# Performance work log

Measured on AMD Instinct MI355X. Metric: run time of the kernel, lower is better.

Reference implementation:

```python
import jax, jax.numpy as jnp
import numpy as np

MAX_REL = 32
NPE = 16
NRBF = 16
KNN = 32

def _layer_norm(x, g, b, eps=1e-5):
    mu = jnp.mean(x, axis=-1, keepdims=True)
    var = jnp.mean((x - mu) ** 2, axis=-1, keepdims=True)
    return (x - mu) * jax.lax.rsqrt(var + eps) * g + b

def _forward(dist_ca, omega, theta, phi, dihedral, mask_angle, mask, S, residue_idx, chain_encoding_all, pos_W, pos_b, edge_W, ln_e_g, ln_e_b, embed_tab, node_W, node_b, ln_n_g, ln_n_b):
    B, L, _ = dist_ca.shape
    # kNN graph from masked CA distances (smallest-K, ascending -> matches torch.topk largest=False)
    D = mask_angle * dist_ca
    D_max = jnp.max(D, axis=-1, keepdims=True)
    D_adjust = D + (1.0 - mask_angle) * D_max
    neg_vals, E_idx = jax.lax.top_k(-D_adjust, KNN)
    D_neighbors = -neg_vals                                     # [B,L,K]
    # 7 pairwise scalar edge channels, gathered at neighbor indices
    offset = (residue_idx[:, :, None] - residue_idx[:, None, :]).astype(jnp.float32)
    feats = jnp.stack([offset, jnp.cos(omega), jnp.sin(omega), jnp.cos(theta), jnp.sin(theta), jnp.cos(phi), jnp.sin(phi)], axis=0)  # [7,B,L,L]
    gathered = jnp.take_along_axis(feats, E_idx[None], axis=3)  # [7,B,L,K]
    edge_s = jax.lax.stop_gradient(gathered).astype(jnp.int32)  # torch .long(): truncate toward zero
    same_chain = (chain_encoding_all[:, :, None] == chain_encoding_all[:, None, :]).astype(jnp.int32)
    E_chains = jnp.take_along_axis(same_chain, E_idx, axis=2)[None]  # [1,B,L,K], broadcasts like tile(7,1,1)
    d = jnp.clip(edge_s + MAX_REL, 0, 2 * MAX_REL) * E_chains + (1 - E_chains) * (2 * MAX_REL + 1)
    E_pos = pos_W[d] + pos_b                                    # one_hot(d,66) @ W == row gather; [7,B,L,K,NPE]
    # rearrange '(n b) l t c -> b l t (n c)'
    E_pos = jnp.transpose(E_pos, (1, 2, 3, 0, 4)).reshape(B, L, KNN, 7 * NPE)
    # RBF of neighbor distances
    mu = jnp.linspace(2.0, 22.0, NRBF)
    sigma = (22.0 - 2.0) / NRBF
    RBF = jnp.exp(-(((D_neighbors[..., None] - mu) / sigma) ** 2))  # [B,L,K,NRBF]
    E = jnp.concatenate([E_pos, RBF], axis=-1) @ edge_W          # [B,L,K,128]
    E = _layer_norm(E, ln_e_g, ln_e_b)
    # node features: embedding(22->6) cat dihedral(6) -> linear(12->128) -> LN
    V = jnp.concatenate([embed_tab[S], dihedral], axis=-1) @ node_W + node_b
    V = _layer_norm(V, ln_n_g, ln_n_b)
    return V, E, E_idx

def setup_inputs():
    key = jax.random.key(0)
    ks = jax.random.split(key, 12)
    B, L, EF = 4, 2048, 128
    inp = {}
    inp["dist_ca"] = jax.random.uniform(ks[0], (B, L, L), jnp.float32) * 20.0 + 2.0
    inp["omega"] = jax.random.normal(ks[1], (B, L, L), jnp.float32)
    inp["theta"] = jax.random.normal(ks[2], (B, L, L), jnp.float32)
    inp["phi"] = jax.random.normal(ks[3], (B, L, L), jnp.float32)
    inp["dihedral"] = jax.random.normal(ks[4], (B, L, 6), jnp.float32)
    inp["mask_angle"] = jnp.ones((B, L, L), jnp.float32)
    inp["mask"] = jnp.ones((B, L), jnp.float32)
    inp["S"] = jax.random.randint(ks[5], (B, L), 0, 22)
    inp["residue_idx"] = jnp.arange(B * L, dtype=jnp.int32).reshape(B, L)
    inp["chain_encoding_all"] = jax.random.randint(ks[6], (B, L), 0, 4)
    # learned parameters (torch Linear weight transposed to [in,out])
    inp["pos_W"] = jax.random.normal(ks[7], (2 * MAX_REL + 2, NPE), jnp.float32) * 0.05
    inp["pos_b"] = jnp.zeros((NPE,), jnp.float32)
    inp["edge_W"] = jax.random.normal(ks[8], (7 * NPE + NRBF, EF), jnp.float32) * 0.05
    inp["ln_e_g"] = jnp.ones((EF,), jnp.float32)
    inp["ln_e_b"] = jnp.zeros((EF,), jnp.float32)
    inp["embed_tab"] = (jax.random.normal(ks[9], (22, 6), jnp.float32) * 0.5).at[21].set(0.0)  # padding_idx=21
    inp["node_W"] = jax.random.normal(ks[10], (12, EF), jnp.float32) * 0.1
    inp["node_b"] = jnp.zeros((EF,), jnp.float32)
    inp["ln_n_g"] = jnp.ones((EF,), jnp.float32)
    inp["ln_n_b"] = jnp.zeros((EF,), jnp.float32)
    return inp

def reference(dist_ca, omega, theta, phi, dihedral, mask_angle, mask, S, residue_idx, chain_encoding_all, pos_W, pos_b, edge_W, ln_e_g, ln_e_b, embed_tab, node_W, node_b, ln_n_g, ln_n_b):
    return _forward(dist_ca, omega, theta, phi, dihedral, mask_angle, mask, S, residue_idx, chain_encoding_all, pos_W, pos_b, edge_W, ln_e_g, ln_e_b, embed_tab, node_W, node_b, ln_n_g, ln_n_b)
```

## Files before the change

kernel.cpp:

```cpp
#include <hip/hip_runtime.h>
#include <hip/hip_bf16.h>
#include <math.h>

namespace {
constexpr int Ln   = 2048;
constexpr int Kn   = 32;
constexpr int EFn  = 128;
constexpr int ROWS = 4 * Ln;
constexpr size_t V_ELEMS = (size_t)ROWS * EFn;
constexpr size_t E_ELEMS = (size_t)ROWS * Kn * EFn;
constexpr size_t IDX_OFF = V_ELEMS + E_ELEMS;

__device__ __forceinline__ unsigned int orderKey(float f) {
  unsigned int u = __float_as_uint(f);
  return (u & 0x80000000u) ? ~u : (u | 0x80000000u);
}
__device__ __forceinline__ float keyToFloat(unsigned int k) {
  unsigned int u = (k & 0x80000000u) ? (k & 0x7fffffffu) : ~k;
  return __uint_as_float(u);
}
__device__ __forceinline__ unsigned long long u64min(unsigned long long a, unsigned long long b) {
  return a < b ? a : b;
}
}

__global__ void pf_tab(const float* __restrict__ pos_W, const float* __restrict__ pos_b,
                       const float* __restrict__ edge_W, float* __restrict__ T) {
  int n = blockIdx.x / 66, dd = blockIdx.x % 66, c = threadIdx.x;
  float acc = 0.f;
#pragma unroll
  for (int m = 0; m < 16; m++)
    acc += (pos_W[dd * 16 + m] + pos_b[m]) * edge_W[(n * 16 + m) * EFn + c];
  T[(size_t)(n * 66 + dd) * EFn + c] = acc;
}

__global__ __launch_bounds__(256) void pf_main(
    const float* __restrict__ dist_ca, const float* __restrict__ omega,
    const float* __restrict__ theta, const float* __restrict__ phi,
    const float* __restrict__ dihedral, const float* __restrict__ mask_angle,
    const int* __restrict__ Sarr, const int* __restrict__ ridx,
    const int* __restrict__ chain, const float* __restrict__ T,
    const float* __restrict__ edge_W, const float* __restrict__ ln_e_g,
    const float* __restrict__ ln_e_b, const float* __restrict__ embed_tab,
    const float* __restrict__ node_W, const float* __restrict__ node_b,
    const float* __restrict__ ln_n_g, const float* __restrict__ ln_n_b,
    float* __restrict__ out) {
  __shared__ unsigned int s_keys[Ln];
  __shared__ unsigned int s_hist[256];
  __shared__ unsigned long long s_cand[64];
  __shared__ unsigned long long s_w64[4];
  __shared__ float s_mx[4], s_mn2[4], s_mx2[4];
  __shared__ float s_v4[4];
  __shared__ int s_nidx[Kn];
  __shared__ float s_nval[Kn];
  __shared__ int s_d7[Kn * 8];
  __shared__ int s_bsel, s_tot, s_cnt;

  const int tid = threadIdx.x;
  const int lane = tid & 63, wid = tid >> 6;
  const int r = blockIdx.x;
  const int b = r >> 11;
  const size_t rowoff = (size_t)r * Ln;

  float Dv[8], Mv[8];
  float lmax = -3.4e38f;
#pragma unroll
  for (int m = 0; m < 8; m++) {
    int j = tid + (m << 8);
    float mk = mask_angle[rowoff + j];
    float dd = mk * dist_ca[rowoff + j];
    Dv[m] = dd; Mv[m] = mk;
    lmax = fmaxf(lmax, dd);
  }
#pragma unroll
  for (int o = 32; o; o >>= 1) lmax = fmaxf(lmax, __shfl_xor(lmax, o));
  if (!lane) s_mx[wid] = lmax;
  __syncthreads();
  const float Dmax = fmaxf(fmaxf(s_mx[0], s_mx[1]), fmaxf(s_mx[2], s_mx[3]));

  float lmin = 3.4e38f; lmax = -3.4e38f;
#pragma unroll
  for (int m = 0; m < 8; m++) {
    float adj = Dv[m] + (1.0f - Mv[m]) * Dmax;
    Dv[m] = adj;
    s_keys[tid + (m << 8)] = orderKey(adj);
    lmin = fminf(lmin, adj); lmax = fmaxf(lmax, adj);
  }
#pragma unroll
  for (int o = 32; o; o >>= 1) {
    lmin = fminf(lmin, __shfl_xor(lmin, o));
    lmax = fmaxf(lmax, __shfl_xor(lmax, o));
  }
  if (!lane) { s_mn2[wid] = lmin; s_mx2[wid] = lmax; }
  s_hist[tid] = 0u;
  __syncthreads();
  const float m0 = fminf(fminf(s_mn2[0], s_mn2[1]), fminf(s_mn2[2], s_mn2[3]));
  const float M0 = fmaxf(fmaxf(s_mx2[0], s_mx2[1]), fmaxf(s_mx2[2], s_mx2[3]));
  const float rng = M0 - m0;
  const float scale = (rng > 0.f) ? 255.0f / rng : 0.f;

  int binv[8];
#pragma unroll
  for (int m = 0; m < 8; m++) {
    int bin = (int)((Dv[m] - m0) * scale);
    bin = bin < 0 ? 0 : (bin > 255 ? 255 : bin);
    binv[m] = bin;
    atomicAdd(&s_hist[bin], 1u);
  }
  __syncthreads();
  for (int off = 1; off < 256; off <<= 1) {
    unsigned int u = 0;
    if (tid >= off) u = s_hist[tid - off];
    __syncthreads();
    if (tid >= off) s_hist[tid] += u;
    __syncthreads();
  }
  {
    unsigned int cum = s_hist[tid];
    unsigned int cump = tid ? s_hist[tid - 1] : 0u;
    if (cum >= (unsigned)Kn && cump < (unsigned)Kn) { s_bsel = tid; s_tot = (int)cum; }
    if (!tid) s_cnt = 0;
  }
  __syncthreads();
  const int bsel = s_bsel;
  const int tot = s_tot;

  if (tot <= 64) {
#pragma unroll
    for (int m = 0; m < 8; m++) {
      if (binv[m] <= bsel) {
        int p = atomicAdd(&s_cnt, 1);
        s_cand[p] = ((unsigned long long)orderKey(Dv[m]) << 16) | (unsigned)(tid + (m << 8));
      }
    }
  }
  __syncthreads();

  if (tot <= 64) {
    if (tid < 64) {
      unsigned long long v = (tid < tot) ? s_cand[tid] : ~0ull;
#pragma unroll
      for (int size = 2; size <= 64; size <<= 1) {
        for (int stride = size >> 1; stride > 0; stride >>= 1) {
          unsigned long long p = __shfl_xor(v, stride);
          bool keepMin = (((tid & stride) == 0) == ((tid & size) == 0));
          v = ((v < p) != keepMin) ? p : v;
        }
      }
      if (tid < Kn) {
        s_nidx[tid] = (int)(v & 0xffffull);
        s_nval[tid] = keyToFloat((unsigned int)(v >> 16));
      }
    }
  } else {
    for (int t = 0; t < Kn; t++) {
      unsigned long long lm = ~0ull;
#pragma unroll
      for (int m = 0; m < 8; m++) {
        int j = tid + (m << 8);
        unsigned long long kk = ((unsigned long long)s_keys[j] << 16) | (unsigned)j;
        lm = u64min(lm, kk);
      }
#pragma unroll
      for (int o = 32; o; o >>= 1) lm = u64min(lm, __shfl_xor(lm, o));
      if (!lane) s_w64[wid] = lm;
      __syncthreads();
      unsigned long long g = u64min(u64min(s_w64[0], s_w64[1]), u64min(s_w64[2], s_w64[3]));
      int j = (int)(g & 0xffffull);
      if (tid == (j & 255)) s_keys[j] = 0xffffffffu;
      if (!tid) { s_nidx[t] = j; s_nval[t] = keyToFloat((unsigned int)(g >> 16)); }
      __syncthreads();
    }
  }
  __syncthreads();

  if (tid < Kn)
    out[IDX_OFF + (size_t)r * Kn + tid] = (float)s_nidx[tid];

  const int ri_i = ridx[r];
  const int ch_i = chain[r];
  if (tid < Kn) {
    int j = s_nidx[tid];
    int rj = ridx[(size_t)b * Ln + j];
    int sc = (ch_i == chain[(size_t)b * Ln + j]) ? 1 : 0;
    int e0 = (int)((float)(ri_i - rj));
    int d0 = e0 + 32; d0 = d0 < 0 ? 0 : (d0 > 64 ? 64 : d0);
    s_d7[tid * 8 + 0] = sc ? d0 : 65;
    size_t pij = rowoff + j;
    float om = omega[pij], th = theta[pij], ph = phi[pij];
    float vals[6] = { cosf(om), sinf(om), cosf(th), sinf(th), cosf(ph), sinf(ph) };
#pragma unroll
    for (int n = 0; n < 6; n++) {
      int e = (int)vals[n];
      int d = e + 32; d = d < 0 ? 0 : (d > 64 ? 64 : d);
      s_d7[tid * 8 + 1 + n] = sc ? d : 65;
    }
  }
  __syncthreads();

  {
    const int k = tid >> 3, sub = tid & 7, c0 = sub << 4;
    float acc[16];
    {
      const float* Tp = T + (size_t)s_d7[k * 8 + 0] * EFn + c0;
#pragma unroll
      for (int m = 0; m < 16; m++) acc[m] = Tp[m];
    }
#pragma unroll
    for (int n = 1; n < 7; n++) {
      const float* Tp = T + (size_t)(n * 66 + s_d7[k * 8 + n]) * EFn + c0;
#pragma unroll
      for (int m = 0; m < 16; m++) acc[m] += Tp[m];
    }
    const float dv = s_nval[k];
#pragma unroll
    for (int rr = 0; rr < 16; rr++) {
      float mu = 2.0f + (20.0f / 15.0f) * (float)rr;
      float t = (dv - mu) * 0.8f;
      float rb = expf(-t * t);
      const float* W2 = edge_W + (size_t)(112 + rr) * EFn + c0;
#pragma unroll
      for (int m = 0; m < 16; m++) acc[m] = fmaf(rb, W2[m], acc[m]);
    }
    float s1 = 0.f, s2 = 0.f;
#pragma unroll
    for (int m = 0; m < 16; m++) { s1 += acc[m]; s2 += acc[m] * acc[m]; }
#pragma unroll
    for (int o = 1; o < 8; o <<= 1) { s1 += __shfl_xor(s1, o); s2 += __shfl_xor(s2, o); }
    const float mean = s1 * (1.0f / 128.0f);
    float var = s2 * (1.0f / 128.0f) - mean * mean;
    var = fmaxf(var, 0.f);
    const float inv = rsqrtf(var + 1e-5f);
    float y[16];
#pragma unroll
    for (int m = 0; m < 16; m++)
      y[m] = (acc[m] - mean) * inv * ln_e_g[c0 + m] + ln_e_b[c0 + m];
    float4* dst = (float4*)(out + V_ELEMS + ((size_t)(r * Kn + k) * EFn + c0));
    dst[0] = make_float4(y[0],  y[1],  y[2],  y[3]);
    dst[1] = make_float4(y[4],  y[5],  y[6],  y[7]);
    dst[2] = make_float4(y[8],  y[9],  y[10], y[11]);
    dst[3] = make_float4(y[12], y[13], y[14], y[15]);
  }

  float a = 0.f;
  if (tid < EFn) {
    const int c = tid;
    const int sv = Sarr[r];
    a = node_b[c];
#pragma unroll
    for (int m = 0; m < 6; m++) a = fmaf(embed_tab[sv * 6 + m], node_W[m * EFn + c], a);
#pragma unroll
    for (int m = 0; m < 6; m++) a = fmaf(dihedral[(size_t)r * 6 + m], node_W[(6 + m) * EFn + c], a);
    float s1 = a, s2 = a * a;
#pragma unroll
    for (int o = 32; o; o >>= 1) { s1 += __shfl_xor(s1, o); s2 += __shfl_xor(s2, o); }
    if (!lane) { s_v4[wid * 2] = s1; s_v4[wid * 2 + 1] = s2; }
  }
  __syncthreads();
  if (tid < EFn) {
    const float S1 = s_v4[0] + s_v4[2], S2 = s_v4[1] + s_v4[3];
    const float mean = S1 * (1.0f / 128.0f);
    float var = S2 * (1.0f / 128.0f) - mean * mean;
    var = fmaxf(var, 0.f);
    const float inv = rsqrtf(var + 1e-5f);
    const float yv = (a - mean) * inv * ln_n_g[tid] + ln_n_b[tid];
    out[(size_t)r * EFn + tid] = yv;
  }
}

extern "C" void kernel_launch(void* const* d_in, const int* in_sizes, int n_in,
                              void* d_out, int out_size, void* d_ws, size_t ws_size,
                              hipStream_t stream) {
  (void)in_sizes; (void)n_in; (void)out_size; (void)ws_size;
  const float* dist_ca    = (const float*)d_in[0];
  const float* omega      = (const float*)d_in[1];
  const float* theta      = (const float*)d_in[2];
  const float* phi        = (const float*)d_in[3];
  const float* dihedral   = (const float*)d_in[4];
  const float* mask_angle = (const float*)d_in[5];
  const int*   S          = (const int*)d_in[7];
  const int*   ridx       = (const int*)d_in[8];
  const int*   chain      = (const int*)d_in[9];
  const float* pos_W      = (const float*)d_in[10];
  const float* pos_b      = (const float*)d_in[11];
  const float* edge_W     = (const float*)d_in[12];
  const float* ln_e_g     = (const float*)d_in[13];
  const float* ln_e_b     = (const float*)d_in[14];
  const float* embed_tab  = (const float*)d_in[15];
  const float* node_W     = (const float*)d_in[16];
  const float* node_b     = (const float*)d_in[17];
  const float* ln_n_g     = (const float*)d_in[18];
  const float* ln_n_b     = (const float*)d_in[19];

  float* T = (float*)d_ws;

  pf_tab<<<7 * 66, 128, 0, stream>>>(pos_W, pos_b, edge_W, T);
  pf_main<<<ROWS, 256, 0, stream>>>(dist_ca, omega, theta, phi, dihedral, mask_angle,
                                    S, ridx, chain, T, edge_W, ln_e_g, ln_e_b,
                                    embed_tab, node_W, node_b, ln_n_g, ln_n_b,
                                    (float*)d_out);
}
```

Measured before the change: 513.3 us.

## Split fused kernel into top-k and edge-feature kernels with vectorized loads

Splits the single per-row kernel into a top-k/node kernel and a separate edge kernel. The top-k kernel hands neighbor metadata to the edge kernel through a packed workspace buffer. The top-k kernel now uses float4 loads, a wave-shuffle prefix scan in place of the barrier-heavy shared scan, and a register valid-mask in place of the shared key array, which cuts LDS use. The edge kernel spreads sin/cos across lanes, shares them by shuffle, and uses __expf. The trade-off is an extra launch, a global round trip for the metadata, and reduced exp precision.

```diff
diff --git a/kernel.cpp b/kernel.cpp
--- a/kernel.cpp
+++ b/kernel.cpp
@@ -10,6 +10,7 @@
 constexpr size_t V_ELEMS = (size_t)ROWS * EFn;
 constexpr size_t E_ELEMS = (size_t)ROWS * Kn * EFn;
 constexpr size_t IDX_OFF = V_ELEMS + E_ELEMS;
+constexpr size_t T_BYTES = (size_t)7 * 66 * EFn * 4;
 
 __device__ __forceinline__ unsigned int orderKey(float f) {
   unsigned int u = __float_as_uint(f);
@@ -34,26 +35,22 @@
   T[(size_t)(n * 66 + dd) * EFn + c] = acc;
 }
 
-__global__ __launch_bounds__(256) void pf_main(
-    const float* __restrict__ dist_ca, const float* __restrict__ omega,
-    const float* __restrict__ theta, const float* __restrict__ phi,
-    const float* __restrict__ dihedral, const float* __restrict__ mask_angle,
-    const int* __restrict__ Sarr, const int* __restrict__ ridx,
-    const int* __restrict__ chain, const float* __restrict__ T,
-    const float* __restrict__ edge_W, const float* __restrict__ ln_e_g,
-    const float* __restrict__ ln_e_b, const float* __restrict__ embed_tab,
-    const float* __restrict__ node_W, const float* __restrict__ node_b,
-    const float* __restrict__ ln_n_g, const float* __restrict__ ln_n_b,
-    float* __restrict__ out) {
-  __shared__ unsigned int s_keys[Ln];
+__global__ __launch_bounds__(256) void pf_topk(
+    const float* __restrict__ dist_ca, const float* __restrict__ mask_angle,
+    const float* __restrict__ dihedral, const int* __restrict__ Sarr,
+    const int* __restrict__ ridx, const int* __restrict__ chain,
+    const float* __restrict__ embed_tab, const float* __restrict__ node_W,
+    const float* __restrict__ node_b, const float* __restrict__ ln_n_g,
+    const float* __restrict__ ln_n_b,
+    uint2* __restrict__ ew, float* __restrict__ out) {
   __shared__ unsigned int s_hist[256];
+  __shared__ unsigned int s_wtot[4];
   __shared__ unsigned long long s_cand[64];
   __shared__ unsigned long long s_w64[4];
   __shared__ float s_mx[4], s_mn2[4], s_mx2[4];
   __shared__ float s_v4[4];
   __shared__ int s_nidx[Kn];
   __shared__ float s_nval[Kn];
-  __shared__ int s_d7[Kn * 8];
   __shared__ int s_bsel, s_tot, s_cnt;
 
   const int tid = threadIdx.x;
@@ -62,19 +59,26 @@
   const int b = r >> 11;
   const size_t rowoff = (size_t)r * Ln;
 
+  const int j0 = tid << 2;
+
   float Dv[8], Mv[8];
+  {
+    float4 da = *(const float4*)(dist_ca + rowoff + j0);
+    float4 db = *(const float4*)(dist_ca + rowoff + 1024 + j0);
+    float4 ma = *(const float4*)(mask_angle + rowoff + j0);
+    float4 mb = *(const float4*)(mask_angle + rowoff + 1024 + j0);
+    Mv[0] = ma.x; Mv[1] = ma.y; Mv[2] = ma.z; Mv[3] = ma.w;
+    Mv[4] = mb.x; Mv[5] = mb.y; Mv[6] = mb.z; Mv[7] = mb.w;
+    Dv[0] = ma.x * da.x; Dv[1] = ma.y * da.y; Dv[2] = ma.z * da.z; Dv[3] = ma.w * da.w;
+    Dv[4] = mb.x * db.x; Dv[5] = mb.y * db.y; Dv[6] = mb.z * db.z; Dv[7] = mb.w * db.w;
+  }
   float lmax = -3.4e38f;
 #pragma unroll
-  for (int m = 0; m < 8; m++) {
-    int j = tid + (m << 8);
-    float mk = mask_angle[rowoff + j];
-    float dd = mk * dist_ca[rowoff + j];
-    Dv[m] = dd; Mv[m] = mk;
-    lmax = fmaxf(lmax, dd);
-  }
+  for (int m = 0; m < 8; m++) lmax = fmaxf(lmax, Dv[m]);
 #pragma unroll
   for (int o = 32; o; o >>= 1) lmax = fmaxf(lmax, __shfl_xor(lmax, o));
   if (!lane) s_mx[wid] = lmax;
+  if (!tid) s_cnt = 0;
   __syncthreads();
   const float Dmax = fmaxf(fmaxf(s_mx[0], s_mx[1]), fmaxf(s_mx[2], s_mx[3]));
 
@@ -83,7 +87,6 @@
   for (int m = 0; m < 8; m++) {
     float adj = Dv[m] + (1.0f - Mv[m]) * Dmax;
     Dv[m] = adj;
-    s_keys[tid + (m << 8)] = orderKey(adj);
     lmin = fminf(lmin, adj); lmax = fmaxf(lmax, adj);
   }
 #pragma unroll
@@ -108,18 +111,24 @@
     atomicAdd(&s_hist[bin], 1u);
   }
   __syncthreads();
-  for (int off = 1; off < 256; off <<= 1) {
-    unsigned int u = 0;
-    if (tid >= off) u = s_hist[tid - off];
+
+  {
+    const unsigned int orig = s_hist[tid];
+    unsigned int v = orig;
+#pragma unroll
+    for (int o = 1; o < 64; o <<= 1) {
+      unsigned int u = __shfl_up(v, o);
+      if (lane >= o) v += u;
+    }
+    if (lane == 63) s_wtot[wid] = v;
     __syncthreads();
-    if (tid >= off) s_hist[tid] += u;
-    __syncthreads();
-  }
-  {
-    unsigned int cum = s_hist[tid];
-    unsigned int cump = tid ? s_hist[tid - 1] : 0u;
-    if (cum >= (unsigned)Kn && cump < (unsigned)Kn) { s_bsel = tid; s_tot = (int)cum; }
-    if (!tid) s_cnt = 0;
+    unsigned int add = 0;
+#pragma unroll
+    for (int w = 0; w < 4; w++) if (w < wid) add += s_wtot[w];
+    const unsigned int cum = v + add;
+    if (cum >= (unsigned)Kn && (cum - orig) < (unsigned)Kn) {
+      s_bsel = tid; s_tot = (int)cum;
+    }
   }
   __syncthreads();
   const int bsel = s_bsel;
@@ -130,13 +139,11 @@
     for (int m = 0; m < 8; m++) {
       if (binv[m] <= bsel) {
         int p = atomicAdd(&s_cnt, 1);
-        s_cand[p] = ((unsigned long long)orderKey(Dv[m]) << 16) | (unsigned)(tid + (m << 8));
+        int j = (m < 4) ? (j0 + m) : (1024 + j0 + m - 4);
+        s_cand[p] = ((unsigned long long)orderKey(Dv[m]) << 16) | (unsigned)j;
       }
     }
-  }
-  __syncthreads();
-
-  if (tot <= 64) {
+    __syncthreads();
     if (tid < 64) {
       unsigned long long v = (tid < tot) ? s_cand[tid] : ~0ull;
 #pragma unroll
@@ -153,13 +160,15 @@
       }
     }
   } else {
+    unsigned int valid = 0xffu;
     for (int t = 0; t < Kn; t++) {
       unsigned long long lm = ~0ull;
 #pragma unroll
       for (int m = 0; m < 8; m++) {
-        int j = tid + (m << 8);
-        unsigned long long kk = ((unsigned long long)s_keys[j] << 16) | (unsigned)j;
-        lm = u64min(lm, kk);
+        if (valid & (1u << m)) {
+          int j = (m < 4) ? (j0 + m) : (1024 + j0 + m - 4);
+          lm = u64min(lm, ((unsigned long long)orderKey(Dv[m]) << 16) | (unsigned)j);
+        }
       }
 #pragma unroll
       for (int o = 32; o; o >>= 1) lm = u64min(lm, __shfl_xor(lm, o));
@@ -167,90 +176,34 @@
       __syncthreads();
       unsigned long long g = u64min(u64min(s_w64[0], s_w64[1]), u64min(s_w64[2], s_w64[3]));
       int j = (int)(g & 0xffffull);
-      if (tid == (j & 255)) s_keys[j] = 0xffffffffu;
+      int owner = (j < 1024) ? (j >> 2) : ((j - 1024) >> 2);
+      if (tid == owner) valid &= ~(1u << ((j < 1024) ? (j & 3) : (4 + (j & 3))));
       if (!tid) { s_nidx[t] = j; s_nval[t] = keyToFloat((unsigned int)(g >> 16)); }
       __syncthreads();
     }
   }
   __syncthreads();
 
-  if (tid < Kn)
-    out[IDX_OFF + (size_t)r * Kn + tid] = (float)s_nidx[tid];
-
-  const int ri_i = ridx[r];
-  const int ch_i = chain[r];
   if (tid < Kn) {
     int j = s_nidx[tid];
+    out[IDX_OFF + (size_t)r * Kn + tid] = (float)j;
     int rj = ridx[(size_t)b * Ln + j];
-    int sc = (ch_i == chain[(size_t)b * Ln + j]) ? 1 : 0;
-    int e0 = (int)((float)(ri_i - rj));
-    int d0 = e0 + 32; d0 = d0 < 0 ? 0 : (d0 > 64 ? 64 : d0);
-    s_d7[tid * 8 + 0] = sc ? d0 : 65;
-    size_t pij = rowoff + j;
-    float om = omega[pij], th = theta[pij], ph = phi[pij];
-    float vals[6] = { cosf(om), sinf(om), cosf(th), sinf(th), cosf(ph), sinf(ph) };
-#pragma unroll
-    for (int n = 0; n < 6; n++) {
-      int e = (int)vals[n];
-      int d = e + 32; d = d < 0 ? 0 : (d > 64 ? 64 : d);
-      s_d7[tid * 8 + 1 + n] = sc ? d : 65;
-    }
-  }
-  __syncthreads();
-
-  {
-    const int k = tid >> 3, sub = tid & 7, c0 = sub << 4;
-    float acc[16];
-    {
-      const float* Tp = T + (size_t)s_d7[k * 8 + 0] * EFn + c0;
-#pragma unroll
-      for (int m = 0; m < 16; m++) acc[m] = Tp[m];
-    }
-#pragma unroll
-    for (int n = 1; n < 7; n++) {
-      const float* Tp = T + (size_t)(n * 66 + s_d7[k * 8 + n]) * EFn + c0;
-#pragma unroll
-      for (int m = 0; m < 16; m++) acc[m] += Tp[m];
-    }
-    const float dv = s_nval[k];
-#pragma unroll
-    for (int rr = 0; rr < 16; rr++) {
-      float mu = 2.0f + (20.0f / 15.0f) * (float)rr;
-      float t = (dv - mu) * 0.8f;
-      float rb = expf(-t * t);
-      const float* W2 = edge_W + (size_t)(112 + rr) * EFn + c0;
-#pragma unroll
-      for (int m = 0; m < 16; m++) acc[m] = fmaf(rb, W2[m], acc[m]);
-    }
-    float s1 = 0.f, s2 = 0.f;
-#pragma unroll
-    for (int m = 0; m < 16; m++) { s1 += acc[m]; s2 += acc[m] * acc[m]; }
-#pragma unroll
-    for (int o = 1; o < 8; o <<= 1) { s1 += __shfl_xor(s1, o); s2 += __shfl_xor(s2, o); }
-    const float mean = s1 * (1.0f / 128.0f);
-    float var = s2 * (1.0f / 128.0f) - mean * mean;
-    var = fmaxf(var, 0.f);
-    const float inv = rsqrtf(var + 1e-5f);
-    float y[16];
-#pragma unroll
-    for (int m = 0; m < 16; m++)
-      y[m] = (acc[m] - mean) * inv * ln_e_g[c0 + m] + ln_e_b[c0 + m];
-    float4* dst = (float4*)(out + V_ELEMS + ((size_t)(r * Kn + k) * EFn + c0));
-    dst[0] = make_float4(y[0],  y[1],  y[2],  y[3]);
-    dst[1] = make_float4(y[4],  y[5],  y[6],  y[7]);
-    dst[2] = make_float4(y[8],  y[9],  y[10], y[11]);
-    dst[3] = make_float4(y[12], y[13], y[14], y[15]);
+    int sc = (chain[r] == chain[(size_t)b * Ln + j]) ? 1 : 0;
+    int d0 = (ridx[r] - rj) + 32;
+    d0 = d0 < 0 ? 0 : (d0 > 64 ? 64 : d0);
+    d0 = sc ? d0 : 65;
+    unsigned int meta = (unsigned)j | ((unsigned)d0 << 11) | ((unsigned)sc << 18);
+    ew[(size_t)r * Kn + tid] = make_uint2(meta, __float_as_uint(s_nval[tid]));
   }
 
   float a = 0.f;
   if (tid < EFn) {
-    const int c = tid;
     const int sv = Sarr[r];
-    a = node_b[c];
-#pragma unroll
-    for (int m = 0; m < 6; m++) a = fmaf(embed_tab[sv * 6 + m], node_W[m * EFn + c], a);
-#pragma unroll
-    for (int m = 0; m < 6; m++) a = fmaf(dihedral[(size_t)r * 6 + m], node_W[(6 + m) * EFn + c], a);
+    a = node_b[tid];
+#pragma unroll
+    for (int m = 0; m < 6; m++) a = fmaf(embed_tab[sv * 6 + m], node_W[m * EFn + tid], a);
+#pragma unroll
+    for (int m = 0; m < 6; m++) a = fmaf(dihedral[(size_t)r * 6 + m], node_W[(6 + m) * EFn + tid], a);
     float s1 = a, s2 = a * a;
 #pragma unroll
     for (int o = 32; o; o >>= 1) { s1 += __shfl_xor(s1, o); s2 += __shfl_xor(s2, o); }
@@ -263,9 +216,82 @@
     float var = S2 * (1.0f / 128.0f) - mean * mean;
     var = fmaxf(var, 0.f);
     const float inv = rsqrtf(var + 1e-5f);
-    const float yv = (a - mean) * inv * ln_n_g[tid] + ln_n_b[tid];
-    out[(size_t)r * EFn + tid] = yv;
-  }
+    out[(size_t)r * EFn + tid] = (a - mean) * inv * ln_n_g[tid] + ln_n_b[tid];
+  }
+}
+
+__global__ __launch_bounds__(256) void pf_edge(
+    const uint2* __restrict__ ew, const float* __restrict__ omega,
+    const float* __restrict__ theta, const float* __restrict__ phi,
+    const float* __restrict__ T, const float* __restrict__ edge_W,
+    const float* __restrict__ ln_e_g, const float* __restrict__ ln_e_b,
+    float* __restrict__ out) {
+  const int tid = threadIdx.x;
+  const int e = blockIdx.x * 32 + (tid >> 3);
+  const int sub = tid & 7, c0 = sub << 4;
+
+  const uint2 md = ew[e];
+  const unsigned meta = md.x;
+  const float dval = __uint_as_float(md.y);
+  const int j = meta & 0x7ff;
+  const int d0 = (meta >> 11) & 0x7f;
+  const int sc = (meta >> 18) & 1;
+  const int r = e >> 5;
+
+  const size_t pij = (size_t)r * Ln + j;
+  float ang = 0.f;
+  if (sub == 0) ang = omega[pij];
+  else if (sub == 1) ang = theta[pij];
+  else if (sub == 2) ang = phi[pij];
+  const float cv = cosf(ang), sv = sinf(ang);
+  const int base = (tid & 63) & ~7;
+  float tr[6];
+  tr[0] = __shfl(cv, base + 0); tr[1] = __shfl(sv, base + 0);
+  tr[2] = __shfl(cv, base + 1); tr[3] = __shfl(sv, base + 1);
+  tr[4] = __shfl(cv, base + 2); tr[5] = __shfl(sv, base + 2);
+
+  float acc[16];
+  {
+    const float* Tp = T + (size_t)d0 * EFn + c0;
+#pragma unroll
+    for (int m = 0; m < 16; m++) acc[m] = Tp[m];
+  }
+#pragma unroll
+  for (int n = 1; n < 7; n++) {
+    int ee = (int)tr[n - 1];
+    int d = ee + 32; d = d < 0 ? 0 : (d > 64 ? 64 : d);
+    d = sc ? d : 65;
+    const float* Tp = T + (size_t)(n * 66 + d) * EFn + c0;
+#pragma unroll
+    for (int m = 0; m < 16; m++) acc[m] += Tp[m];
+  }
+#pragma unroll
+  for (int rr = 0; rr < 16; rr++) {
+    float mu = 2.0f + (20.0f / 15.0f) * (float)rr;
+    float t = (dval - mu) * 0.8f;
+    float rb = __expf(-t * t);
+    const float* W2 = edge_W + (size_t)(112 + rr) * EFn + c0;
+#pragma unroll
+    for (int m = 0; m < 16; m++) acc[m] = fmaf(rb, W2[m], acc[m]);
+  }
+  float s1 = 0.f, s2 = 0.f;
+#pragma unroll
+  for (int m = 0; m < 16; m++) { s1 += acc[m]; s2 += acc[m] * acc[m]; }
+#pragma unroll
+  for (int o = 1; o < 8; o <<= 1) { s1 += __shfl_xor(s1, o); s2 += __shfl_xor(s2, o); }
+  const float mean = s1 * (1.0f / 128.0f);
+  float var = s2 * (1.0f / 128.0f) - mean * mean;
+  var = fmaxf(var, 0.f);
+  const float inv = rsqrtf(var + 1e-5f);
+  float y[16];
+#pragma unroll
+  for (int m = 0; m < 16; m++)
+    y[m] = (acc[m] - mean) * inv * ln_e_g[c0 + m] + ln_e_b[c0 + m];
+  float4* dst = (float4*)(out + V_ELEMS + ((size_t)e * EFn + c0));
+  dst[0] = make_float4(y[0],  y[1],  y[2],  y[3]);
+  dst[1] = make_float4(y[4],  y[5],  y[6],  y[7]);
+  dst[2] = make_float4(y[8],  y[9],  y[10], y[11]);
+  dst[3] = make_float4(y[12], y[13], y[14], y[15]);
 }
 
 extern "C" void kernel_launch(void* const* d_in, const int* in_sizes, int n_in,
@@ -292,11 +318,13 @@
   const float* ln_n_g     = (const float*)d_in[18];
   const float* ln_n_b     = (const float*)d_in[19];
 
-  float* T = (float*)d_ws;
+  float* T  = (float*)d_ws;
+  uint2* ew = (uint2*)((char*)d_ws + T_BYTES);
 
   pf_tab<<<7 * 66, 128, 0, stream>>>(pos_W, pos_b, edge_W, T);
-  pf_main<<<ROWS, 256, 0, stream>>>(dist_ca, omega, theta, phi, dihedral, mask_angle,
-                                    S, ridx, chain, T, edge_W, ln_e_g, ln_e_b,
+  pf_topk<<<ROWS, 256, 0, stream>>>(dist_ca, mask_angle, dihedral, S, ridx, chain,
                                     embed_tab, node_W, node_b, ln_n_g, ln_n_b,
-                                    (float*)d_out);
-}
+                                    ew, (float*)d_out);
+  pf_edge<<<ROWS * Kn / 32, 256, 0, stream>>>(ew, omega, theta, phi, T, edge_W,
+                                              ln_e_g, ln_e_b, (float*)d_out);
+}
```

Result: slower. 529.1 us (+3.1%).
